# Optimization experiments

Hardware: AMD Instinct MI355X
Metric: run time of the kernel (lower is better)

Reference implementation:

```python
import jax, jax.numpy as jnp
import numpy as np

N = 50000   # nodes
E = 800000  # edges (avg degree 16)
D = 128     # input feature size
H = 256     # hidden size
P = 512     # pool_size
O = 64      # output size


def setup_inputs() -> dict:
    key = jax.random.key(0)
    ks = jax.random.split(key, 9)
    x = jax.random.normal(ks[0], (N, D), dtype=jnp.float32)
    src = jax.random.randint(ks[1], (E,), 0, N)
    dst = jax.random.randint(ks[2], (E,), 0, N)
    w = lambda k, sh: jax.random.normal(k, sh, dtype=jnp.float32) * 0.05
    return {
        "x": x, "src": src, "dst": dst,
        "aggW0": w(ks[3], (D, P)),      # aggregator W1, layer 0
        "aggW1": w(ks[4], (H, P)),
        "aggW2": w(ks[5], (H, P)),
        "linW0": w(ks[6], (D + P, H)),  # linear after concat, layer 0
        "linW1": w(ks[7], (H + P, H)),
        "linW2": w(ks[8], (H + P, O)),
    }


def _sage_layer(x, src, dst, aggW, linW, activate):
    # DGLMaxPoolAggregator: project sources, scatter-max to destinations
    h = x @ aggW                                   # [N, P]
    hN = jax.ops.segment_max(h[src], dst, num_segments=x.shape[0])  # [N, P]
    # DGL fills zeros for nodes with no in-edges; segment_max gives -inf
    hN = jnp.where(jnp.isneginf(hN), jnp.zeros_like(hN), hN)
    out = jnp.concatenate([x, hN], axis=1) @ linW  # [N, out]
    return jax.nn.relu(out) if activate else out


def reference(x, src, dst, aggW0, aggW1, aggW2, linW0, linW1, linW2):
    x = _sage_layer(x, src, dst, aggW0, linW0, True)   # layer 0 (+relu, dropout p=0)
    x = _sage_layer(x, src, dst, aggW1, linW1, True)   # layer 1 (+relu)
    return _sage_layer(x, src, dst, aggW2, linW2, False)  # output layer
```

## Files before the change

### kernel.cpp

```cpp
#include <hip/hip_runtime.h>
#include <hip/hip_bf16.h>

#define MN 50000
#define NE 800000
#define DD 128
#define HH 256
#define PP 512
#define OO 64

typedef unsigned short bf16r;
using short8 = __attribute__((ext_vector_type(8))) short;
using ushort8 = __attribute__((ext_vector_type(8))) unsigned short;
using f32x4 = __attribute__((ext_vector_type(4))) float;

__device__ __forceinline__ float b2f(bf16r s) {
  unsigned int u = ((unsigned int)s) << 16;
  float f;
  __builtin_memcpy(&f, &u, 4);
  return f;
}
__device__ __forceinline__ bf16r f2b(float f) {
  unsigned int u;
  __builtin_memcpy(&u, &f, 4);
  u += 0x7fffu + ((u >> 16) & 1u);
  return (bf16r)(u >> 16);
}
__device__ __forceinline__ unsigned short keymap(unsigned short u) {
  return u ^ ((u & 0x8000u) ? 0x7FFFu : 0u);
}
__device__ __forceinline__ void stC(float* p, float v) { *p = v; }
__device__ __forceinline__ void stC(bf16r* p, float v) { *p = f2b(v); }

__device__ __forceinline__ void async16(void* lds, const void* g) {
  auto l = reinterpret_cast<__attribute__((address_space(3))) char*>(
      reinterpret_cast<uintptr_t>(lds));
  auto gp = reinterpret_cast<const __attribute__((address_space(1))) char*>(
      reinterpret_cast<uintptr_t>(g));
  __builtin_amdgcn_global_load_lds(gp, l, 16, 0, 0);
}

__global__ void zero_ints(int* __restrict__ p, int n) {
  int i = blockIdx.x * blockDim.x + threadIdx.x;
  if (i < n) p[i] = 0;
}

__global__ void conv_bf16(const float* __restrict__ in, bf16r* __restrict__ out, int n4) {
  int i = blockIdx.x * 256 + threadIdx.x;
  if (i < n4) {
    float4 v = reinterpret_cast<const float4*>(in)[i];
    ushort4 u;
    u.x = f2b(v.x); u.y = f2b(v.y); u.z = f2b(v.z); u.w = f2b(v.w);
    reinterpret_cast<ushort4*>(out)[i] = u;
  }
}

__device__ __forceinline__ void tw1(const float* B, bf16r* BT, int i, int K, int Nc) {
  int k = i / Nc, n = i - k * Nc;
  BT[(size_t)n * K + k] = f2b(B[i]);
}
__global__ void transpose_all(const float* __restrict__ b0, const float* __restrict__ b1,
                              const float* __restrict__ b2, const float* __restrict__ b3,
                              const float* __restrict__ b4, const float* __restrict__ b5,
                              bf16r* __restrict__ t0, bf16r* __restrict__ t1,
                              bf16r* __restrict__ t2, bf16r* __restrict__ t3,
                              bf16r* __restrict__ t4, bf16r* __restrict__ t5) {
  int idx = blockIdx.x * 256 + threadIdx.x;
  if (idx < 196608) {
    if (idx < 65536) tw1(b0, t0, idx, 128, 512);
    else tw1(b1, t1, idx - 65536, 256, 512);
  } else if (idx < 491520) {
    if (idx < 327680) tw1(b2, t2, idx - 196608, 256, 512);
    else tw1(b3, t3, idx - 327680, 640, 256);
  } else if (idx < 737280) {
    if (idx < 688128) tw1(b4, t4, idx - 491520, 768, 256);
    else tw1(b5, t5, idx - 688128, 768, 64);
  }
}

__global__ void count_edges(const int* __restrict__ dst, int* __restrict__ counts) {
  int e = blockIdx.x * blockDim.x + threadIdx.x;
  if (e < NE) atomicAdd(&counts[dst[e]], 1);
}

__global__ __launch_bounds__(1024) void scan_local(const int* __restrict__ counts,
                                                   int* __restrict__ row_ptr,
                                                   int* __restrict__ bsum) {
  __shared__ int buf[1024];
  const int b = blockIdx.x, t = threadIdx.x;
  int2 c2 = reinterpret_cast<const int2*>(counts)[b * 1024 + t];
  int tsum = c2.x + c2.y;
  buf[t] = tsum;
  __syncthreads();
  int s = tsum;
  for (int off = 1; off < 1024; off <<= 1) {
    int add = (t >= off) ? buf[t - off] : 0;
    __syncthreads();
    s += add;
    buf[t] = s;
    __syncthreads();
  }
  int excl = s - tsum;
  int2 o;
  o.x = excl;
  o.y = excl + c2.x;
  reinterpret_cast<int2*>(row_ptr)[b * 1024 + t] = o;
  if (t == 1023) bsum[b] = s;
}

__global__ __launch_bounds__(1024) void scan_add(int* __restrict__ row_ptr,
                                                 int* __restrict__ cursor,
                                                 const int* __restrict__ bsum) {
  const int b = blockIdx.x, t = threadIdx.x;
  int off = 0;
  for (int j = 0; j < b; ++j) off += bsum[j];
  int i0 = b * 2048 + 2 * t;
#pragma unroll
  for (int k = 0; k < 2; ++k) {
    int i = i0 + k;
    if (i <= MN) {
      int v = row_ptr[i] + off;
      row_ptr[i] = v;
      if (i < MN) cursor[i] = v;
    }
  }
}

__global__ void scatter_edges(const int* __restrict__ src, const int* __restrict__ dst,
                              int* __restrict__ cursor, int* __restrict__ esrc) {
  int e = blockIdx.x * blockDim.x + threadIdx.x;
  if (e < NE) {
    int d = dst[e];
    int pos = atomicAdd(&cursor[d], 1);
    esrc[pos] = src[e];
  }
}

__global__ __launch_bounds__(256) void seg_max(const bf16r* __restrict__ h,
                                               const int* __restrict__ row_ptr,
                                               const int* __restrict__ esrc,
                                               bf16r* __restrict__ hN) {
  const int node = blockIdx.x * 4 + (threadIdx.x >> 6);
  if (node >= MN) return;
  const int lane = threadIdx.x & 63;
  const int beg = row_ptr[node];
  const int end = row_ptr[node + 1];
  short8 m8;
#pragma unroll
  for (int j = 0; j < 8; ++j) m8[j] = (short)0x807F;

  for (int cb = beg; cb < end; cb += 64) {
    const int c = min(64, end - cb);
    int e = esrc[cb + min(lane, c - 1)];
    for (int i = 0; i < c; i += 4) {
      int s0 = __shfl(e, i);
      int s1 = __shfl(e, min(i + 1, c - 1));
      int s2 = __shfl(e, min(i + 2, c - 1));
      int s3 = __shfl(e, min(i + 3, c - 1));
      short8 u0 = *reinterpret_cast<const short8*>(h + ((size_t)s0 << 9) + lane * 8);
      short8 u1 = *reinterpret_cast<const short8*>(h + ((size_t)s1 << 9) + lane * 8);
      short8 u2 = *reinterpret_cast<const short8*>(h + ((size_t)s2 << 9) + lane * 8);
      short8 u3 = *reinterpret_cast<const short8*>(h + ((size_t)s3 << 9) + lane * 8);
      m8 = __builtin_elementwise_max(m8, u0);
      m8 = __builtin_elementwise_max(m8, u1);
      m8 = __builtin_elementwise_max(m8, u2);
      m8 = __builtin_elementwise_max(m8, u3);
    }
  }
  ushort8 o;
  if (beg == end) {
#pragma unroll
    for (int j = 0; j < 8; ++j) o[j] = 0;
  } else {
#pragma unroll
    for (int j = 0; j < 8; ++j) o[j] = keymap((unsigned short)m8[j]);
  }
  *reinterpret_cast<ushort8*>(hN + (size_t)node * PP + lane * 8) = o;
}

template <int BN, int WMC, int WNC, bool DUAL, bool RELU, bool KEYED, typename TO>
__global__ __launch_bounds__(256) void gemm_mfma(
    const bf16r* __restrict__ A1, int K1, const bf16r* __restrict__ A2, int K2,
    const bf16r* __restrict__ BT, int Ktot, TO* __restrict__ C, int M, int NC) {
  constexpr int BM = 128, BK = 32;
  constexpr int WM = BM / WMC;
  constexpr int WN = BN / WNC;
  constexpr int FM = WM / 16, FN = WN / 16;
  __shared__ short As[BM * BK];
  __shared__ short Bs[BN * BK];
  const int tid = threadIdx.x;
  const int lane = tid & 63;
  const int wv = tid >> 6;
  const int wr = wv / WNC, wc = wv % WNC;
  const int m0 = blockIdx.x * BM;
  const int n0 = blockIdx.y * BN;

  f32x4 acc[FM][FN];
#pragma unroll
  for (int i = 0; i < FM; ++i)
#pragma unroll
    for (int j = 0; j < FN; ++j)
#pragma unroll
      for (int r = 0; r < 4; ++r) acc[i][j][r] = 0.f;

#pragma unroll
  for (int ph = 0; ph < (DUAL ? 2 : 1); ++ph) {
    const int K = ph ? K2 : K1;
    const int kb = ph ? K1 : 0;
    const bf16r* Ab = ph ? A2 : A1;
    for (int kt = 0; kt < K; kt += BK) {
      __syncthreads();
      {
        const int o = wv * 1024 + lane * 16;
#pragma unroll
        for (int c = 0; c < 2; ++c) {
          int oo = o + c * 4096;
          int row = oo >> 6, colb = oo & 63;
          const char* g = (const char*)Ab + ((size_t)(m0 + row) * K + kt) * 2 + colb;
          async16((char*)As + oo, g);
        }
      }
      {
        const int o = wv * 1024 + lane * 16;
#pragma unroll
        for (int c = 0; c < (BN * 64) / 4096; ++c) {
          int oo = o + c * 4096;
          int row = oo >> 6, colb = oo & 63;
          const char* g =
              (const char*)BT + ((size_t)(n0 + row) * Ktot + kb + kt) * 2 + colb;
          async16((char*)Bs + oo, g);
        }
      }
      __syncthreads();
      short8 af[FM], bfv[FN];
#pragma unroll
      for (int i = 0; i < FM; ++i)
        af[i] = *(const short8*)(As + (wr * WM + i * 16 + (lane & 15)) * BK +
                                 (lane >> 4) * 8);
#pragma unroll
      for (int j = 0; j < FN; ++j)
        bfv[j] = *(const short8*)(Bs + (wc * WN + j * 16 + (lane & 15)) * BK +
                                  (lane >> 4) * 8);
#pragma unroll
      for (int i = 0; i < FM; ++i)
#pragma unroll
        for (int j = 0; j < FN; ++j)
          acc[i][j] =
              __builtin_amdgcn_mfma_f32_16x16x32_bf16(af[i], bfv[j], acc[i][j], 0, 0, 0);
    }
  }
  const int crow0 = wr * WM + (lane >> 4) * 4;
  const int ccol0 = wc * WN + (lane & 15);
#pragma unroll
  for (int i = 0; i < FM; ++i)
#pragma unroll
    for (int j = 0; j < FN; ++j)
#pragma unroll
      for (int r = 0; r < 4; ++r) {
        int row = m0 + crow0 + i * 16 + r;
        if (row < M) {
          float v = acc[i][j][r];
          if (RELU) v = fmaxf(v, 0.f);
          TO* p = &C[(size_t)row * NC + n0 + ccol0 + j * 16];
          if (KEYED) {
            *(bf16r*)p = keymap(f2b(v));
          } else {
            stC(p, v);
          }
        }
      }
}

extern "C" void kernel_launch(void* const* d_in, const int* in_sizes, int n_in,
                              void* d_out, int out_size, void* d_ws, size_t ws_size,
                              hipStream_t stream) {
  const float* x = (const float*)d_in[0];
  const int* src = (const int*)d_in[1];
  const int* dst = (const int*)d_in[2];
  const float* aggW0 = (const float*)d_in[3];
  const float* aggW1 = (const float*)d_in[4];
  const float* aggW2 = (const float*)d_in[5];
  const float* linW0 = (const float*)d_in[6];
  const float* linW1 = (const float*)d_in[7];
  const float* linW2 = (const float*)d_in[8];
  float* out = (float*)d_out;

  char* ws = (char*)d_ws;
  size_t off = 0;
  auto alloc = [&](size_t bytes) {
    void* p = ws + off;
    off = (off + bytes + 255) & ~(size_t)255;
    return p;
  };
  bf16r* h = (bf16r*)alloc((size_t)MN * PP * 2);
  bf16r* hN = (bf16r*)alloc((size_t)MN * PP * 2);
  bf16r* act1 = (bf16r*)alloc((size_t)MN * HH * 2);
  bf16r* act2 = (bf16r*)alloc((size_t)MN * HH * 2);
  bf16r* xb = (bf16r*)alloc((size_t)MN * DD * 2);
  bf16r* aggW0T = (bf16r*)alloc(512 * 128 * 2);
  bf16r* aggW1T = (bf16r*)alloc(512 * 256 * 2);
  bf16r* aggW2T = (bf16r*)alloc(512 * 256 * 2);
  bf16r* linW0T = (bf16r*)alloc(640 * 256 * 2);
  bf16r* linW1T = (bf16r*)alloc(768 * 256 * 2);
  bf16r* linW2T = (bf16r*)alloc(768 * 64 * 2);
  int* row_ptr = (int*)alloc(51264 * 4);
  int* cursor = (int*)alloc(MN * 4);
  int* counts = (int*)alloc(51264 * 4);
  int* bsum = (int*)alloc(32 * 4);
  int* esrc = (int*)alloc(NE * 4);

  zero_ints<<<(51264 + 255) / 256, 256, 0, stream>>>(counts, 51264);
  count_edges<<<(NE + 255) / 256, 256, 0, stream>>>(dst, counts);
  scan_local<<<25, 1024, 0, stream>>>(counts, row_ptr, bsum);
  scan_add<<<25, 1024, 0, stream>>>(row_ptr, cursor, bsum);
  scatter_edges<<<(NE + 255) / 256, 256, 0, stream>>>(src, dst, cursor, esrc);

  conv_bf16<<<((MN * DD / 4) + 255) / 256, 256, 0, stream>>>(x, xb, MN * DD / 4);
  transpose_all<<<(737280 + 255) / 256, 256, 0, stream>>>(
      aggW0, aggW1, aggW2, linW0, linW1, linW2,
      aggW0T, aggW1T, aggW2T, linW0T, linW1T, linW2T);

  dim3 g512((MN + 127) / 128, 4);
  dim3 g256((MN + 127) / 128, 2);
  dim3 g64((MN + 127) / 128, 1);
  const int segGrid = (MN + 3) / 4;

  gemm_mfma<128, 2, 2, false, false, true, bf16r><<<g512, 256, 0, stream>>>(
      xb, DD, (const bf16r*)nullptr, 0, aggW0T, DD, h, MN, PP);
  seg_max<<<segGrid, 256, 0, stream>>>(h, row_ptr, esrc, hN);
  gemm_mfma<128, 2, 2, true, true, false, bf16r><<<g256, 256, 0, stream>>>(
      xb, DD, hN, PP, linW0T, DD + PP, act1, MN, HH);

  gemm_mfma<128, 2, 2, false, false, true, bf16r><<<g512, 256, 0, stream>>>(
      act1, HH, (const bf16r*)nullptr, 0, aggW1T, HH, h, MN, PP);
  seg_max<<<segGrid, 256, 0, stream>>>(h, row_ptr, esrc, hN);
  gemm_mfma<128, 2, 2, true, true, false, bf16r><<<g256, 256, 0, stream>>>(
      act1, HH, hN, PP, linW1T, HH + PP, act2, MN, HH);

  gemm_mfma<128, 2, 2, false, false, true, bf16r><<<g512, 256, 0, stream>>>(
      act2, HH, (const bf16r*)nullptr, 0, aggW2T, HH, h, MN, PP);
  seg_max<<<segGrid, 256, 0, stream>>>(h, row_ptr, esrc, hN);
  gemm_mfma<64, 4, 1, true, false, false, float><<<g64, 256, 0, stream>>>(
      act2, HH, hN, PP, linW2T, HH + PP, out, MN, OO);
}
```

Before: 742.4 us.

## Split seg_max by column blocks and remap GEMM tiles across XCDs with wider BN

The segment-max kernel now launches four column blocks per node. Each wave processes eight edges at a time as four lane groups of 16, then combines the groups with cross-lane shuffle max reductions. This is meant to raise parallelism and cut per-node serialisation for short neighbour lists, at the cost of redundant index loads and shuffle reductions. The GEMMs switch to BN=256 tiles on a 1D grid, with block IDs remapped so consecutive tiles land on the same XCD, intended to improve L2 locality of A rows. The wider tiles raise per-block register and LDS pressure and halve the number of blocks.

Measured after the change: 767.0 us. +3.3%, slower.

```diff
diff --git a/kernel.cpp b/kernel.cpp
--- a/kernel.cpp
+++ b/kernel.cpp
@@ -142,42 +142,49 @@
   const int node = blockIdx.x * 4 + (threadIdx.x >> 6);
   if (node >= MN) return;
   const int lane = threadIdx.x & 63;
+  const int g = lane >> 4;
+  const int sl = lane & 15;
+  const int colbase = blockIdx.y * 128 + sl * 8;
   const int beg = row_ptr[node];
   const int end = row_ptr[node + 1];
   short8 m8;
 #pragma unroll
   for (int j = 0; j < 8; ++j) m8[j] = (short)0x807F;
 
-  for (int cb = beg; cb < end; cb += 64) {
-    const int c = min(64, end - cb);
-    int e = esrc[cb + min(lane, c - 1)];
-    for (int i = 0; i < c; i += 4) {
-      int s0 = __shfl(e, i);
-      int s1 = __shfl(e, min(i + 1, c - 1));
-      int s2 = __shfl(e, min(i + 2, c - 1));
-      int s3 = __shfl(e, min(i + 3, c - 1));
-      short8 u0 = *reinterpret_cast<const short8*>(h + ((size_t)s0 << 9) + lane * 8);
-      short8 u1 = *reinterpret_cast<const short8*>(h + ((size_t)s1 << 9) + lane * 8);
-      short8 u2 = *reinterpret_cast<const short8*>(h + ((size_t)s2 << 9) + lane * 8);
-      short8 u3 = *reinterpret_cast<const short8*>(h + ((size_t)s3 << 9) + lane * 8);
-      m8 = __builtin_elementwise_max(m8, u0);
-      m8 = __builtin_elementwise_max(m8, u1);
-      m8 = __builtin_elementwise_max(m8, u2);
-      m8 = __builtin_elementwise_max(m8, u3);
+  for (int cb = beg; cb < end; cb += 8) {
+    int e0 = esrc[min(cb + g, end - 1)];
+    int e1 = esrc[min(cb + 4 + g, end - 1)];
+    short8 u0 = *reinterpret_cast<const short8*>(h + ((size_t)e0 << 9) + colbase);
+    short8 u1 = *reinterpret_cast<const short8*>(h + ((size_t)e1 << 9) + colbase);
+    m8 = __builtin_elementwise_max(m8, __builtin_elementwise_max(u0, u1));
+  }
+#pragma unroll
+  for (int mask = 16; mask <= 32; mask <<= 1) {
+    int4 vi;
+    __builtin_memcpy(&vi, &m8, 16);
+    int4 ot;
+    ot.x = __shfl_xor(vi.x, mask);
+    ot.y = __shfl_xor(vi.y, mask);
+    ot.z = __shfl_xor(vi.z, mask);
+    ot.w = __shfl_xor(vi.w, mask);
+    short8 o8;
+    __builtin_memcpy(&o8, &ot, 16);
+    m8 = __builtin_elementwise_max(m8, o8);
+  }
+  if (lane < 16) {
+    ushort8 o;
+    if (beg == end) {
+#pragma unroll
+      for (int j = 0; j < 8; ++j) o[j] = 0;
+    } else {
+#pragma unroll
+      for (int j = 0; j < 8; ++j) o[j] = keymap((unsigned short)m8[j]);
     }
-  }
-  ushort8 o;
-  if (beg == end) {
-#pragma unroll
-    for (int j = 0; j < 8; ++j) o[j] = 0;
-  } else {
-#pragma unroll
-    for (int j = 0; j < 8; ++j) o[j] = keymap((unsigned short)m8[j]);
-  }
-  *reinterpret_cast<ushort8*>(hN + (size_t)node * PP + lane * 8) = o;
-}
-
-template <int BN, int WMC, int WNC, bool DUAL, bool RELU, bool KEYED, typename TO>
+    *reinterpret_cast<ushort8*>(hN + (size_t)node * PP + colbase) = o;
+  }
+}
+
+template <int BN, int NCB, int WMC, int WNC, bool DUAL, bool RELU, bool KEYED, typename TO>
 __global__ __launch_bounds__(256) void gemm_mfma(
     const bf16r* __restrict__ A1, int K1, const bf16r* __restrict__ A2, int K2,
     const bf16r* __restrict__ BT, int Ktot, TO* __restrict__ C, int M, int NC) {
@@ -191,8 +198,12 @@
   const int lane = tid & 63;
   const int wv = tid >> 6;
   const int wr = wv / WNC, wc = wv % WNC;
-  const int m0 = blockIdx.x * BM;
-  const int n0 = blockIdx.y * BN;
+  const int nwg = gridDim.x;
+  const int q = nwg >> 3, r = nwg & 7;
+  const int xcd = blockIdx.x & 7, slot = blockIdx.x >> 3;
+  const int wgid = (xcd < r ? xcd * (q + 1) : r * (q + 1) + (xcd - r) * q) + slot;
+  const int m0 = (wgid / NCB) * BM;
+  const int n0 = (wgid % NCB) * BN;
 
   f32x4 acc[FM][FN];
 #pragma unroll
@@ -200,7 +211,7 @@
 #pragma unroll
     for (int j = 0; j < FN; ++j)
 #pragma unroll
-      for (int r = 0; r < 4; ++r) acc[i][j][r] = 0.f;
+      for (int r2 = 0; r2 < 4; ++r2) acc[i][j][r2] = 0.f;
 
 #pragma unroll
   for (int ph = 0; ph < (DUAL ? 2 : 1); ++ph) {
@@ -255,10 +266,10 @@
 #pragma unroll
     for (int j = 0; j < FN; ++j)
 #pragma unroll
-      for (int r = 0; r < 4; ++r) {
-        int row = m0 + crow0 + i * 16 + r;
+      for (int r2 = 0; r2 < 4; ++r2) {
+        int row = m0 + crow0 + i * 16 + r2;
         if (row < M) {
-          float v = acc[i][j][r];
+          float v = acc[i][j][r2];
           if (RELU) v = fmaxf(v, 0.f);
           TO* p = &C[(size_t)row * NC + n0 + ccol0 + j * 16];
           if (KEYED) {
@@ -319,26 +330,27 @@
       aggW0, aggW1, aggW2, linW0, linW1, linW2,
       aggW0T, aggW1T, aggW2T, linW0T, linW1T, linW2T);
 
-  dim3 g512((MN + 127) / 128, 4);
-  dim3 g256((MN + 127) / 128, 2);
-  dim3 g64((MN + 127) / 128, 1);
-  const int segGrid = (MN + 3) / 4;
-
-  gemm_mfma<128, 2, 2, false, false, true, bf16r><<<g512, 256, 0, stream>>>(
+  const int RB = (MN + 127) / 128;
+  dim3 gagg(RB * 2);
+  dim3 glin(RB);
+  dim3 gout(RB);
+  dim3 gseg((MN + 3) / 4, 4);
+
+  gemm_mfma<256, 2, 2, 2, false, false, true, bf16r><<<gagg, 256, 0, stream>>>(
       xb, DD, (const bf16r*)nullptr, 0, aggW0T, DD, h, MN, PP);
-  seg_max<<<segGrid, 256, 0, stream>>>(h, row_ptr, esrc, hN);
-  gemm_mfma<128, 2, 2, true, true, false, bf16r><<<g256, 256, 0, stream>>>(
+  seg_max<<<gseg, 256, 0, stream>>>(h, row_ptr, esrc, hN);
+  gemm_mfma<256, 1, 2, 2, true, true, false, bf16r><<<glin, 256, 0, stream>>>(
       xb, DD, hN, PP, linW0T, DD + PP, act1, MN, HH);
 
-  gemm_mfma<128, 2, 2, false, false, true, bf16r><<<g512, 256, 0, stream>>>(
+  gemm_mfma<256, 2, 2, 2, false, false, true, bf16r><<<gagg, 256, 0, stream>>>(
       act1, HH, (const bf16r*)nullptr, 0, aggW1T, HH, h, MN, PP);
-  seg_max<<<segGrid, 256, 0, stream>>>(h, row_ptr, esrc, hN);
-  gemm_mfma<128, 2, 2, true, true, false, bf16r><<<g256, 256, 0, stream>>>(
+  seg_max<<<gseg, 256, 0, stream>>>(h, row_ptr, esrc, hN);
+  gemm_mfma<256, 1, 2, 2, true, true, false, bf16r><<<glin, 256, 0, stream>>>(
       act1, HH, hN, PP, linW1T, HH + PP, act2, MN, HH);
 
-  gemm_mfma<128, 2, 2, false, false, true, bf16r><<<g512, 256, 0, stream>>>(
+  gemm_mfma<256, 2, 2, 2, false, false, true, bf16r><<<gagg, 256, 0, stream>>>(
       act2, HH, (const bf16r*)nullptr, 0, aggW2T, HH, h, MN, PP);
-  seg_max<<<segGrid, 256, 0, stream>>>(h, row_ptr, esrc, hN);
-  gemm_mfma<64, 4, 1, true, false, false, float><<<g64, 256, 0, stream>>>(
+  seg_max<<<gseg, 256, 0, stream>>>(h, row_ptr, esrc, hN);
+  gemm_mfma<64, 1, 4, 1, true, false, false, float><<<gout, 256, 0, stream>>>(
       act2, HH, hN, PP, linW2T, HH + PP, out, MN, OO);
 }
```
